# Performance work log

Hardware: AMD Instinct MI355X
Metric: run time of the kernel (lower is better)

## Reference

```python
import jax, jax.numpy as jnp
import numpy as np

B, T, OBS, ACT, H, OUT, NLAYERS = 4096, 50, 64, 16, 256, 64, 5


def setup_inputs() -> dict:
    key = jax.random.key(0)
    ks = jax.random.split(key, 8)
    w = 0.05
    return {
        "trajectory": jax.random.normal(ks[0], (B, T, OBS), dtype=jnp.float32),
        "actions": jax.random.normal(ks[1], (B, T, ACT), dtype=jnp.float32),
        "Wi": jax.random.normal(ks[2], (OBS + ACT, 4 * H), dtype=jnp.float32) * w,
        "Wh": jax.random.normal(ks[3], (H, 4 * H), dtype=jnp.float32) * w,
        "bh": jnp.zeros((4 * H,), dtype=jnp.float32),
        "mlp_W": jax.random.normal(ks[4], (NLAYERS, H, H), dtype=jnp.float32) * w,
        "mlp_b": jnp.zeros((NLAYERS, H), dtype=jnp.float32),
        "Wout": jax.random.normal(ks[5], (H, OUT), dtype=jnp.float32) * w,
        "bout": jnp.zeros((OUT,), dtype=jnp.float32),
    }


def reference(trajectory, actions, Wi, Wh, bh, mlp_W, mlp_b, Wout, bout):
    # Features extractor = flatten (identity for 1D sensor obs); preprocess is identity for Box.
    x = jnp.concatenate([trajectory, actions], axis=-1)  # [B, T, OBS+ACT]
    xs = jnp.swapaxes(x, 0, 1)  # [T, B, D] for scan over time

    hdim = Wh.shape[0]
    c0 = jnp.zeros((x.shape[0], hdim), dtype=x.dtype)
    h0 = jnp.zeros((x.shape[0], hdim), dtype=x.dtype)

    def step(carry, xt):
        c, h = carry
        z = xt @ Wi + h @ Wh + bh  # [B, 4H]
        zi, zf, zg, zo = jnp.split(z, 4, axis=-1)
        i = jax.nn.sigmoid(zi)
        f = jax.nn.sigmoid(zf)
        g = jax.nn.silu(zg)  # activation_fn=nn.silu
        o = jax.nn.sigmoid(zo)
        c_new = f * c + i * g
        h_new = o * jax.nn.silu(c_new)
        return (c_new, h_new), None

    (c, h), _ = jax.lax.scan(step, (c0, h0), xs)

    out = h
    for k in range(mlp_W.shape[0]):
        out = jax.nn.silu(out @ mlp_W[k] + mlp_b[k])
    pred = out @ Wout + bout
    return pred
```

## Files before the change

kernel.cpp:

```cpp
#include <hip/hip_runtime.h>
#include <hip/hip_fp16.h>


typedef _Float16 h8 __attribute__((ext_vector_type(8)));
typedef _Float16 hv4 __attribute__((ext_vector_type(4)));
typedef float f4 __attribute__((ext_vector_type(4)));

#define NB    4096
#define TSEQ  50
#define DOBS  64
#define DACT  16
#define HD    256
#define DOUT  64
#define NL    5

#define NKT   11
#define AROW  360
#define MTILE 16
#define NWG   (NB / MTILE)
#define NTHR  512

#define WS_MLP   (704 * 512)
#define WS_WOUT  (WS_MLP + 640 * 512)

#define LDS_AS     (MTILE * AROW)
#define LDS_WCOFF  (2 * LDS_AS)
#define WCB        16
#define LDS_HALVES (LDS_WCOFF + 8 * WCB * 512)
#define LDS_BYTES  (LDS_HALVES * 2)
static_assert(LDS_BYTES <= 160 * 1024, "LDS overflow");

#define SB_P     8
#define NSTREAM  48

__device__ __forceinline__ void lds_barrier() {
  asm volatile("s_waitcnt lgkmcnt(0)\n\ts_barrier" ::: "memory");
}

__device__ __forceinline__ float sigf(float x) {
  const float e = __builtin_amdgcn_exp2f(x * -1.44269504088896f);
  return __builtin_amdgcn_rcpf(1.f + e);
}

__device__ constexpr int soff(int c) {
  if (c < 44) { const int g = c & 3, kt = c >> 2; return ((g * 16 + 1) * NKT + kt) * 512; }
  const int g = c - 44; return ((g * 16) * NKT + 10) * 512;
}

__global__ void __launch_bounds__(256) repack_kernel(
    const float* __restrict__ Wi, const float* __restrict__ Wh,
    const float* __restrict__ mlpW, const float* __restrict__ Wout,
    _Float16* __restrict__ wsW)
{
  const int gt  = blockIdx.x * 256 + threadIdx.x;
  const int gb  = gt >> 6;
  const int l   = gt & 63;
  const int l15 = l & 15;
  const int kb  = (l >> 4) * 8;
  h8 v;
  if (gb < 704) {
    const int nt = gb / NKT, kt = gb - nt * NKT;
    const int n  = nt * 16 + l15;
#pragma unroll
    for (int j = 0; j < 8; ++j) {
      const int k = kt * 32 + kb + j;
      float s = 0.f;
      if (k < 80)       s = Wi[k * 1024 + n];
      else if (k < 336) s = Wh[(k - 80) * 1024 + n];
      v[j] = (_Float16)s;
    }
  } else if (gb < 1344) {
    const int b2 = gb - 704;
    const int L  = b2 >> 7, rr = b2 & 127;
    const int nt = rr >> 3, kt = rr & 7;
    const int n  = nt * 16 + l15;
#pragma unroll
    for (int j = 0; j < 8; ++j) {
      const int k = kt * 32 + kb + j;
      v[j] = (_Float16)mlpW[(size_t)L * 65536 + k * 256 + n];
    }
  } else {
    const int b3 = gb - 1344;
    const int nt = b3 >> 3, kt = b3 & 7;
    const int n  = nt * 16 + l15;
#pragma unroll
    for (int j = 0; j < 8; ++j) {
      const int k = kt * 32 + kb + j;
      v[j] = (_Float16)Wout[k * 64 + n];
    }
  }
  *(h8*)&wsW[(size_t)gb * 512 + l * 8] = v;
}

__global__ void __launch_bounds__(NTHR, 2) lstm_kernel(
    const float* __restrict__ traj, const float* __restrict__ acts,
    const float* __restrict__ bh,   const float* __restrict__ mlpb,
    const float* __restrict__ bout, const _Float16* __restrict__ wsW,
    float* __restrict__ out)
{
  extern __shared__ __align__(16) _Float16 lds[];
  _Float16* As0 = lds;
  _Float16* As1 = lds + LDS_AS;
  _Float16* Wc  = lds + LDS_WCOFF;

  const int tid = threadIdx.x;
  const int w   = tid >> 6;
  const int l   = tid & 63;
  const int l15 = l & 15;
  const int lq  = l >> 4;
  const int rbase = blockIdx.x * MTILE;

  for (int i = tid; i < 2 * LDS_AS; i += NTHR) lds[i] = (_Float16)0.f;

#pragma unroll
  for (int j = 0; j < WCB; ++j) {
    const int g = j & 3, kt = 6 + (j >> 2);
    const h8 v = *(const h8*)&wsW[(size_t)((g * 16 + w * 2) * NKT + kt) * 512 + l * 8];
    *(h8*)&Wc[(w * WCB + j) * 512 + l * 8] = v;
  }

  h8 rw[24];
#pragma unroll
  for (int kt = 0; kt < 6; ++kt)
#pragma unroll
    for (int g = 0; g < 4; ++g)
      rw[kt * 4 + g] = *(const h8*)&wsW[(size_t)((g * 16 + w * 2) * NKT + kt) * 512 + l * 8];

  float c[2][4];
#pragma unroll
  for (int cb = 0; cb < 2; ++cb)
#pragma unroll
    for (int r = 0; r < 4; ++r) c[cb][r] = 0.f;

  float bias[4][2];
#pragma unroll
  for (int g = 0; g < 4; ++g) {
    bias[g][0] = bh[g * 256 + w * 32 + l15];
    bias[g][1] = bh[g * 256 + w * 32 + 16 + l15];
  }

  __syncthreads();

  if (tid < 256) {
    const int r = tid >> 4, q = tid & 15;
    const float4 v = *(const float4*)&traj[(size_t)(rbase + r) * (TSEQ * DOBS) + q * 4];
    hv4 hx = { (_Float16)v.x, (_Float16)v.y, (_Float16)v.z, (_Float16)v.w };
    *(hv4*)&As0[r * AROW + q * 4] = hx;
  } else {
    const int r = (tid - 256) >> 4, q = (tid - 256) & 15;
    As0[r * AROW + 64 + q] = (_Float16)acts[(size_t)(rbase + r) * (TSEQ * DACT) + q];
  }
  __syncthreads();

  unsigned long long wbits = (unsigned long long)(const void*)wsW;

  h8 sb[SB_P];
  {
    const _Float16* wlb0 = wsW + (size_t)(w * 2 * NKT) * 512 + l * 8;
#pragma unroll
    for (int cc = 0; cc < SB_P; ++cc) sb[cc] = *(const h8*)&wlb0[soff(cc)];
  }

  auto step = [&](int t, const _Float16* buf, _Float16* nbuf) {
    asm volatile("" : "+s"(wbits) : : "memory");
    const _Float16* wst = (const _Float16*)wbits;
    const _Float16* wlb = wst + (size_t)(w * 2 * NKT) * 512 + l * 8;

    float4 xv; float xa;
    const bool havex = (t + 1 < TSEQ);
    if (havex) {
      if (tid < 256) {
        const int r = tid >> 4, q = tid & 15;
        xv = *(const float4*)&traj[(size_t)(rbase + r) * (TSEQ * DOBS) + (t + 1) * DOBS + q * 4];
      } else {
        const int r = (tid - 256) >> 4, q = (tid - 256) & 15;
        xa = acts[(size_t)(rbase + r) * (TSEQ * DACT) + (t + 1) * DACT + q];
      }
    }

    f4 acc0[4], acc1[4];
#pragma unroll
    for (int g = 0; g < 4; ++g) {
      acc0[g] = f4{0.f, 0.f, 0.f, 0.f};
      acc1[g] = f4{0.f, 0.f, 0.f, 0.f};
    }

#pragma unroll
    for (int kt = 0; kt < NKT; ++kt) {
      const h8 a0 = *(const h8*)&buf[l15 * AROW + kt * 32 + lq * 8];
#pragma unroll
      for (int g = 0; g < 4; ++g) {
        h8 bf0;
        if (kt < 6)       bf0 = rw[kt * 4 + g];
        else if (kt < 10) bf0 = *(const h8*)&Wc[(w * WCB + (kt - 6) * 4 + g) * 512 + l * 8];
        else              bf0 = sb[4 + g];
        acc0[g] = __builtin_amdgcn_mfma_f32_16x16x32_f16(a0, bf0, acc0[g], 0, 0, 0);

        const int cc = kt * 4 + g;
        acc1[g] = __builtin_amdgcn_mfma_f32_16x16x32_f16(a0, sb[cc % SB_P], acc1[g], 0, 0, 0);
        sb[cc % SB_P] = *(const h8*)&wlb[soff((cc + SB_P) % NSTREAM)];
        if (kt == 10) {
          sb[4 + g] = *(const h8*)&wlb[soff(4 + g)];
        }
      }
    }

    {
      const int colh = 80 + w * 32 + l15;
#pragma unroll
      for (int r = 0; r < 4; ++r) {
        const float zi = acc0[0][r] + bias[0][0];
        const float zf = acc0[1][r] + bias[1][0];
        const float zg = acc0[2][r] + bias[2][0];
        const float zo = acc0[3][r] + bias[3][0];
        const float ig = sigf(zi), fg = sigf(zf), og = sigf(zo);
        const float gg = zg * sigf(zg);
        const float cn = fg * c[0][r] + ig * gg;
        c[0][r] = cn;
        nbuf[(lq * 4 + r) * AROW + colh] = (_Float16)(og * cn * sigf(cn));
      }
    }
    {
      const int colh = 80 + w * 32 + 16 + l15;
#pragma unroll
      for (int r = 0; r < 4; ++r) {
        const float zi = acc1[0][r] + bias[0][1];
        const float zf = acc1[1][r] + bias[1][1];
        const float zg = acc1[2][r] + bias[2][1];
        const float zo = acc1[3][r] + bias[3][1];
        const float ig = sigf(zi), fg = sigf(zf), og = sigf(zo);
        const float gg = zg * sigf(zg);
        const float cn = fg * c[1][r] + ig * gg;
        c[1][r] = cn;
        nbuf[(lq * 4 + r) * AROW + colh] = (_Float16)(og * cn * sigf(cn));
      }
    }

    if (havex) {
      if (tid < 256) {
        const int r = tid >> 4, q = tid & 15;
        hv4 hx = { (_Float16)xv.x, (_Float16)xv.y, (_Float16)xv.z, (_Float16)xv.w };
        *(hv4*)&nbuf[r * AROW + q * 4] = hx;
      } else {
        const int r = (tid - 256) >> 4, q = (tid - 256) & 15;
        nbuf[r * AROW + 64 + q] = (_Float16)xa;
      }
    }
  };

#pragma unroll 1
  for (int t = 0; t < TSEQ; t += 2) {
    step(t, As0, As1);
    lds_barrier();
    step(t + 1, As1, As0);
    lds_barrier();
  }

  for (int i = tid; i < MTILE * HD; i += NTHR) {
    const int r = i >> 8, cc = i & 255;
    As1[r * AROW + cc] = As0[r * AROW + 80 + cc];
  }
  __syncthreads();

#pragma unroll 1
  for (int L = 0; L < NL; ++L) {
    const _Float16* in = (L & 1) ? As0 : As1;
    _Float16*       ob = (L & 1) ? As1 : As0;
    const _Float16* wl = wsW + WS_MLP + (size_t)L * (128 * 512);
    float bcol[2];
    bcol[0] = mlpb[L * HD + w * 32 + l15];
    bcol[1] = mlpb[L * HD + w * 32 + 16 + l15];

    f4 acc[2];
    acc[0] = f4{0.f, 0.f, 0.f, 0.f};
    acc[1] = f4{0.f, 0.f, 0.f, 0.f};
#pragma unroll
    for (int kt = 0; kt < 8; ++kt) {
      const h8 a0 = *(const h8*)&in[l15 * AROW + kt * 32 + lq * 8];
#pragma unroll
      for (int cb = 0; cb < 2; ++cb) {
        const h8 bf = *(const h8*)&wl[(size_t)((w * 2 + cb) * 8 + kt) * 512 + l * 8];
        acc[cb] = __builtin_amdgcn_mfma_f32_16x16x32_f16(a0, bf, acc[cb], 0, 0, 0);
      }
    }
#pragma unroll
    for (int cb = 0; cb < 2; ++cb)
#pragma unroll
      for (int r = 0; r < 4; ++r) {
        const float z = acc[cb][r] + bcol[cb];
        ob[(lq * 4 + r) * AROW + w * 32 + cb * 16 + l15] = (_Float16)(z * sigf(z));
      }
    __syncthreads();
  }

  if (w < 4) {
    const _Float16* wo = wsW + WS_WOUT;
    const float bo = bout[w * 16 + l15];
    f4 acc0 = f4{0.f, 0.f, 0.f, 0.f};
#pragma unroll
    for (int kt = 0; kt < 8; ++kt) {
      const h8 a0 = *(const h8*)&As0[l15 * AROW + kt * 32 + lq * 8];
      const h8 bf = *(const h8*)&wo[(size_t)(w * 8 + kt) * 512 + l * 8];
      acc0 = __builtin_amdgcn_mfma_f32_16x16x32_f16(a0, bf, acc0, 0, 0, 0);
    }
#pragma unroll
    for (int r = 0; r < 4; ++r)
      out[(size_t)(rbase + lq * 4 + r) * DOUT + w * 16 + l15] = acc0[r] + bo;
  }
}

extern "C" void kernel_launch(void* const* d_in, const int* in_sizes, int n_in,
                              void* d_out, int out_size, void* d_ws, size_t ws_size,
                              hipStream_t stream)
{
  const float* traj = (const float*)d_in[0];
  const float* acts = (const float*)d_in[1];
  const float* Wi   = (const float*)d_in[2];
  const float* Wh   = (const float*)d_in[3];
  const float* bh   = (const float*)d_in[4];
  const float* mlpW = (const float*)d_in[5];
  const float* mlpb = (const float*)d_in[6];
  const float* Wout = (const float*)d_in[7];
  const float* bout = (const float*)d_in[8];
  _Float16* wsW = (_Float16*)d_ws;

  (void)hipFuncSetAttribute((const void*)lstm_kernel,
                            hipFuncAttributeMaxDynamicSharedMemorySize, LDS_BYTES);

  repack_kernel<<<344, 256, 0, stream>>>(Wi, Wh, mlpW, Wout, wsW);
  lstm_kernel<<<NWG, NTHR, LDS_BYTES, stream>>>(traj, acts, bh, mlpb, bout, wsW, (float*)d_out);
}
```

Before: 321.6 us.

## Stream kt=5 gate weights from global and merge sigmoid reciprocals in LSTM cell

The register-resident weight block shrinks from 6 to 5 k-tiles, and the kt=5 block for column block 0 joins the global-memory weight stream. The stream ring grows to 13 slots over 52 entries with a new offset map. The gate math now combines pairs of sigmoid reciprocals (i*g and o*silu(c)) into single rcp calls on products, which removes two rcp per element. This frees VGPRs and cuts transcendental work, at the cost of more global loads per step inside the recurrence and possible overflow when the exp products grow large.

```diff
diff --git a/kernel.cpp b/kernel.cpp
--- a/kernel.cpp
+++ b/kernel.cpp
@@ -30,21 +30,22 @@
 #define LDS_BYTES  (LDS_HALVES * 2)
 static_assert(LDS_BYTES <= 160 * 1024, "LDS overflow");
 
-#define SB_P     8
-#define NSTREAM  48
+#define SB_P     13
+#define NSTREAM  52
 
 __device__ __forceinline__ void lds_barrier() {
   asm volatile("s_waitcnt lgkmcnt(0)\n\ts_barrier" ::: "memory");
 }
 
-__device__ __forceinline__ float sigf(float x) {
-  const float e = __builtin_amdgcn_exp2f(x * -1.44269504088896f);
-  return __builtin_amdgcn_rcpf(1.f + e);
-}
-
 __device__ constexpr int soff(int c) {
-  if (c < 44) { const int g = c & 3, kt = c >> 2; return ((g * 16 + 1) * NKT + kt) * 512; }
-  const int g = c - 44; return ((g * 16) * NKT + 10) * 512;
+  int kt, cbb, g;
+  if (c < 20)      { kt = c >> 2;              cbb = 1; g = c & 3; }
+  else if (c < 24) { kt = 5;                   cbb = 0; g = c - 20; }
+  else if (c < 28) { kt = 5;                   cbb = 1; g = c - 24; }
+  else if (c < 44) { kt = 6 + ((c - 28) >> 2); cbb = 1; g = (c - 28) & 3; }
+  else if (c < 48) { kt = 10;                  cbb = 0; g = c - 44; }
+  else             { kt = 10;                  cbb = 1; g = c - 48; }
+  return ((g * 16 + cbb) * NKT + kt) * 512;
 }
 
 __global__ void __launch_bounds__(256) repack_kernel(
@@ -119,9 +120,9 @@
     *(h8*)&Wc[(w * WCB + j) * 512 + l * 8] = v;
   }
 
-  h8 rw[24];
-#pragma unroll
-  for (int kt = 0; kt < 6; ++kt)
+  h8 rw[20];
+#pragma unroll
+  for (int kt = 0; kt < 5; ++kt)
 #pragma unroll
     for (int g = 0; g < 4; ++g)
       rw[kt * 4 + g] = *(const h8*)&wsW[(size_t)((g * 16 + w * 2) * NKT + kt) * 512 + l * 8];
@@ -190,21 +191,24 @@
       const h8 a0 = *(const h8*)&buf[l15 * AROW + kt * 32 + lq * 8];
 #pragma unroll
       for (int g = 0; g < 4; ++g) {
-        h8 bf0;
-        if (kt < 6)       bf0 = rw[kt * 4 + g];
-        else if (kt < 10) bf0 = *(const h8*)&Wc[(w * WCB + (kt - 6) * 4 + g) * 512 + l * 8];
-        else              bf0 = sb[4 + g];
-        acc0[g] = __builtin_amdgcn_mfma_f32_16x16x32_f16(a0, bf0, acc0[g], 0, 0, 0);
-
-        const int cc = kt * 4 + g;
-        acc1[g] = __builtin_amdgcn_mfma_f32_16x16x32_f16(a0, sb[cc % SB_P], acc1[g], 0, 0, 0);
-        sb[cc % SB_P] = *(const h8*)&wlb[soff((cc + SB_P) % NSTREAM)];
-        if (kt == 10) {
-          sb[4 + g] = *(const h8*)&wlb[soff(4 + g)];
+        if (kt < 5) {
+          acc0[g] = __builtin_amdgcn_mfma_f32_16x16x32_f16(a0, rw[kt * 4 + g], acc0[g], 0, 0, 0);
+        } else if (kt >= 6 && kt <= 9) {
+          const h8 bf0 = *(const h8*)&Wc[(w * WCB + (kt - 6) * 4 + g) * 512 + l * 8];
+          acc0[g] = __builtin_amdgcn_mfma_f32_16x16x32_f16(a0, bf0, acc0[g], 0, 0, 0);
+        } else {
+          const int c0 = (kt == 5) ? (20 + g) : (44 + g);
+          acc0[g] = __builtin_amdgcn_mfma_f32_16x16x32_f16(a0, sb[c0 % SB_P], acc0[g], 0, 0, 0);
+          sb[c0 % SB_P] = *(const h8*)&wlb[soff((c0 + SB_P) % NSTREAM)];
         }
-      }
-    }
-
+
+        const int c1 = kt * 4 + g + (kt >= 5 ? 4 : 0) + (kt >= 10 ? 4 : 0);
+        acc1[g] = __builtin_amdgcn_mfma_f32_16x16x32_f16(a0, sb[c1 % SB_P], acc1[g], 0, 0, 0);
+        sb[c1 % SB_P] = *(const h8*)&wlb[soff((c1 + SB_P) % NSTREAM)];
+      }
+    }
+
+    const float KE = -1.44269504088896f;
     {
       const int colh = 80 + w * 32 + l15;
 #pragma unroll
@@ -213,11 +217,17 @@
         const float zf = acc0[1][r] + bias[1][0];
         const float zg = acc0[2][r] + bias[2][0];
         const float zo = acc0[3][r] + bias[3][0];
-        const float ig = sigf(zi), fg = sigf(zf), og = sigf(zo);
-        const float gg = zg * sigf(zg);
-        const float cn = fg * c[0][r] + ig * gg;
+        const float ei = __builtin_amdgcn_exp2f(zi * KE);
+        const float ef = __builtin_amdgcn_exp2f(zf * KE);
+        const float eg = __builtin_amdgcn_exp2f(zg * KE);
+        const float eo = __builtin_amdgcn_exp2f(zo * KE);
+        const float fg = __builtin_amdgcn_rcpf(1.f + ef);
+        const float igg = zg * __builtin_amdgcn_rcpf((1.f + ei) * (1.f + eg));
+        const float cn = fg * c[0][r] + igg;
         c[0][r] = cn;
-        nbuf[(lq * 4 + r) * AROW + colh] = (_Float16)(og * cn * sigf(cn));
+        const float ec = __builtin_amdgcn_exp2f(cn * KE);
+        const float hn = cn * __builtin_amdgcn_rcpf((1.f + eo) * (1.f + ec));
+        nbuf[(lq * 4 + r) * AROW + colh] = (_Float16)hn;
       }
     }
     {
@@ -228,11 +238,17 @@
         const float zf = acc1[1][r] + bias[1][1];
         const float zg = acc1[2][r] + bias[2][1];
         const float zo = acc1[3][r] + bias[3][1];
-        const float ig = sigf(zi), fg = sigf(zf), og = sigf(zo);
-        const float gg = zg * sigf(zg);
-        const float cn = fg * c[1][r] + ig * gg;
+        const float ei = __builtin_amdgcn_exp2f(zi * KE);
+        const float ef = __builtin_amdgcn_exp2f(zf * KE);
+        const float eg = __builtin_amdgcn_exp2f(zg * KE);
+        const float eo = __builtin_amdgcn_exp2f(zo * KE);
+        const float fg = __builtin_amdgcn_rcpf(1.f + ef);
+        const float igg = zg * __builtin_amdgcn_rcpf((1.f + ei) * (1.f + eg));
+        const float cn = fg * c[1][r] + igg;
         c[1][r] = cn;
-        nbuf[(lq * 4 + r) * AROW + colh] = (_Float16)(og * cn * sigf(cn));
+        const float ec = __builtin_amdgcn_exp2f(cn * KE);
+        const float hn = cn * __builtin_amdgcn_rcpf((1.f + eo) * (1.f + ec));
+        nbuf[(lq * 4 + r) * AROW + colh] = (_Float16)hn;
       }
     }
 
@@ -288,7 +304,9 @@
 #pragma unroll
       for (int r = 0; r < 4; ++r) {
         const float z = acc[cb][r] + bcol[cb];
-        ob[(lq * 4 + r) * AROW + w * 32 + cb * 16 + l15] = (_Float16)(z * sigf(z));
+        const float ez = __builtin_amdgcn_exp2f(z * -1.44269504088896f);
+        ob[(lq * 4 + r) * AROW + w * 32 + cb * 16 + l15] =
+            (_Float16)(z * __builtin_amdgcn_rcpf(1.f + ez));
       }
     __syncthreads();
   }
```

New measurement: 335.0 us. 4.2% more time.
